# Kernel optimization log

Hardware: AMD Instinct MI355X
Metric: run time of the kernel (lower is better)

Reference implementation:

```python
import jax, jax.numpy as jnp
import numpy as np

B, N, OBJ_DIM, Q_DIM, KSIZE = 128, 36, 2048, 1024, 8
HID = Q_DIM // 2  # 512, inter_dim for obj_method='mul'
MID = Q_DIM // 4  # 256


def wn_linear(x, v, g, b):
    # weight_norm: W = g * v / ||v||_row
    w = v * (g / jnp.linalg.norm(v, axis=1))[:, None]
    return x @ w.T + b


def setup_inputs() -> dict:
    key = jax.random.key(0)
    ks = jax.random.split(key, 8)
    node_feats = jax.random.normal(ks[0], (B, N, OBJ_DIM), dtype=jnp.float32)
    q_feats = jax.random.normal(ks[1], (B, Q_DIM), dtype=jnp.float32)
    # off-diagonal (self-loops removed) flat indices into the (B*N*N,) pairwise tensor
    grid = np.arange(N * N).reshape(N, N)
    per = grid[~np.eye(N, dtype=bool)]            # (N*(N-1),)
    idx = (np.arange(B)[:, None] * (N * N) + per[None, :]).reshape(-1)
    indexes = jnp.asarray(idx, dtype=jnp.int64)
    s = 0.02
    return {
        "node_feats": node_feats,
        "q_feats": q_feats,
        "indexes": indexes,
        "v_obj": jax.random.normal(ks[2], (HID, OBJ_DIM), jnp.float32) * s,
        "g_obj": jnp.ones((HID,), jnp.float32),
        "b_obj": jnp.zeros((HID,), jnp.float32),
        "v_q": jax.random.normal(ks[3], (HID, Q_DIM), jnp.float32) * s,
        "g_q": jnp.ones((HID,), jnp.float32),
        "b_q": jnp.zeros((HID,), jnp.float32),
        "v_l1": jax.random.normal(ks[4], (MID, HID), jnp.float32) * s,
        "g_l1": jnp.ones((MID,), jnp.float32),
        "b_l1": jnp.zeros((MID,), jnp.float32),
        "v_l2": jax.random.normal(ks[5], (KSIZE, MID), jnp.float32) * s,
        "g_l2": jnp.ones((KSIZE,), jnp.float32),
        "b_l2": jnp.zeros((KSIZE,), jnp.float32),
    }


def reference(node_feats, q_feats, indexes, v_obj, g_obj, b_obj, v_q, g_q, b_q,
              v_l1, g_l1, b_l1, v_l2, g_l2, b_l2):
    b, n, _ = node_feats.shape
    nf = wn_linear(node_feats, v_obj, g_obj, b_obj)        # (b, n, HID)
    # decode flat pairwise index -> (batch, i, j); node_intersect 'mul' then gather
    bi = indexes // (n * n)
    rem = indexes % (n * n)
    i, j = rem // n, rem % n
    obj_feats = nf[bi, i] * nf[bi, j]                       # (m, HID)
    m = indexes.shape[0]
    qp = wn_linear(q_feats, v_q, g_q, b_q)                  # (b, HID)
    q_re = jnp.repeat(qp, m // b, axis=0)                   # (m, HID)
    edge_feats = obj_feats * q_re
    h = jax.nn.relu(wn_linear(edge_feats, v_l1, g_l1, b_l1))
    return wn_linear(h, v_l2, g_l2, b_l2)                   # (m, KSIZE)
```

## Files before the change

kernel.cpp:

```cpp
#include <hip/hip_runtime.h>
#include <hip/hip_fp16.h>

typedef __attribute__((ext_vector_type(8))) _Float16 half8;
typedef __attribute__((ext_vector_type(2))) __fp16 fp16x2;
typedef __attribute__((ext_vector_type(4))) float f32x4;
typedef unsigned short u16;
typedef unsigned int u32;

__device__ __forceinline__ u16 f2h(float f) {
  union { _Float16 h; u16 u; } cv; cv.h = (_Float16)f; return cv.u;
}

__device__ __forceinline__ u32 pkrtz(float a, float b) {
  union { fp16x2 h; u32 u; } cv;
  cv.h = __builtin_amdgcn_cvt_pkrtz(a, b);
  return cv.u;
}

__device__ __forceinline__ f32x4 mfma16h(half8 a, half8 b, f32x4 c) {
  return __builtin_amdgcn_mfma_f32_16x16x32_f16(a, b, c, 0, 0, 0);
}

__device__ __forceinline__ void gload_lds16(const void* g, void* l) {
  __builtin_amdgcn_global_load_lds(
      (const __attribute__((address_space(1))) void*)g,
      (__attribute__((address_space(3))) void*)l, 16, 0, 0);
}

__device__ __forceinline__ half8 ldh8(const char* p) {
  union { half8 h; int4 v; } r; r.v = *(const int4*)p; return r.h;
}

__device__ __forceinline__ uint4 pkmul4(uint4 x, uint4 y) {
  union U { uint4 v; __half2 h[4]; };
  U X, Y, E; X.v = x; Y.v = y;
  #pragma unroll
  for (int i = 0; i < 4; i++) E.h[i] = __hmul2(X.h[i], Y.h[i]);
  return E.v;
}
__device__ __forceinline__ half8 as_h8(uint4 v) {
  union { uint4 v; half8 h; } r; r.v = v; return r.h;
}

__device__ __forceinline__ void wn_row(const float* __restrict__ v,
                                       const float* __restrict__ g,
                                       int K, int Nreal, u16* __restrict__ outW,
                                       int row, int l) {
  if (row >= Nreal) {
    for (int k = l; k < K; k += 64) outW[row * K + k] = 0;
    return;
  }
  const float* vr = v + (size_t)row * K;
  float ss = 0.f;
  for (int k = l * 4; k < K; k += 256) {
    f32x4 x = *(const f32x4*)(vr + k);
    ss += x.x * x.x + x.y * x.y + x.z * x.z + x.w * x.w;
  }
  #pragma unroll
  for (int m = 32; m >= 1; m >>= 1) ss += __shfl_xor(ss, m, 64);
  const float scale = g[row] / sqrtf(ss);
  for (int k = l; k < K; k += 64) outW[row * K + k] = f2h(vr[k] * scale);
}

__global__ __launch_bounds__(256) void prep(
    const float* __restrict__ node, u16* __restrict__ node_h,
    const float* __restrict__ qf, u16* __restrict__ q_h,
    const float* __restrict__ v_obj, const float* __restrict__ g_obj,
    const float* __restrict__ v_q,   const float* __restrict__ g_q,
    const float* __restrict__ v_l1,  const float* __restrict__ g_l1,
    const float* __restrict__ v_l2,  const float* __restrict__ g_l2,
    u16* __restrict__ Wobjh, u16* __restrict__ Wqh,
    u16* __restrict__ W1f,   u16* __restrict__ W2p,
    const int* __restrict__ indexes, int* __restrict__ posPair,
    int* __restrict__ ij_tab) {
  const int b = blockIdx.x;
  if (b < 4672) {
    const int i = (b * 256 + threadIdx.x) * 8;
    const float* in; u16* out; int off;
    if (i < 9437184) { in = node; out = node_h; off = i; }
    else             { in = qf;   out = q_h;    off = i - 9437184; }
    f32x4 a = *(const f32x4*)(in + off);
    f32x4 c = *(const f32x4*)(in + off + 4);
    uint4 r;
    r.x = pkrtz(a.x, a.y); r.y = pkrtz(a.z, a.w);
    r.z = pkrtz(c.x, c.y); r.w = pkrtz(c.z, c.w);
    *(uint4*)(out + off) = r;
    return;
  }
  const int sub = threadIdx.x >> 6, l = threadIdx.x & 63;
  const int b2 = b - 4672;
  if (b2 < 128) {
    wn_row(v_obj, g_obj, 2048, 512, Wobjh, b2 * 4 + sub, l);
  } else if (b2 < 256) {
    wn_row(v_q, g_q, 1024, 512, Wqh, (b2 - 128) * 4 + sub, l);
  } else if (b2 < 320) {
    const int row = (b2 - 256) * 4 + sub;
    const float* vr = v_l1 + (size_t)row * 512;
    float ss = 0.f;
    for (int k = l * 4; k < 512; k += 256) {
      f32x4 x = *(const f32x4*)(vr + k);
      ss += x.x * x.x + x.y * x.y + x.z * x.z + x.w * x.w;
    }
    #pragma unroll
    for (int m = 32; m >= 1; m >>= 1) ss += __shfl_xor(ss, m, 64);
    const float scale = g_l1[row] / sqrtf(ss);
    const int swz = (row >> 1) & 3;
    for (int c = l; c < 512; c += 64) {
      const int kc = c >> 5, col = c & 31, q = col >> 3, e = col & 7;
      W1f[kc * 8192 + row * 32 + ((q ^ swz) << 3) + e] = f2h(vr[c] * scale);
    }
  } else if (b2 < 324) {
    wn_row(v_l2, g_l2, 256, 8, W2p, (b2 - 320) * 4 + sub, l);
  } else {
    const int m = (b2 - 324) * 256 + threadIdx.x;
    if (m < 161280) {
      const int idx = indexes[m];
      const int bi = idx / 1296;
      const int rem = idx - bi * 1296;
      const int i = rem / 36, j = rem - i * 36;
      const int i2 = (i < j) ? i : j, j2 = (i < j) ? j : i;
      const int p = i2 * (71 - i2) / 2 + (j2 - i2 - 1);
      posPair[(bi * 640 + p) * 2 + ((i < j) ? 0 : 1)] = m;
    } else {
      const int u = m - 161280;
      if (u < 1296) {
        const int i = u / 36, j = u - i * 36;
        if (i < j) ij_tab[i * (71 - i) / 2 + (j - i - 1)] = u;
      } else if (u < 1306) {
        ij_tab[630 + (u - 1296)] = 35 * 36 + 35;
      }
    }
  }
}

__global__ __launch_bounds__(256, 3) void gemm_merged(
    const u16* __restrict__ node_h, const u16* __restrict__ Wobjh,
    const float* __restrict__ b_obj, u16* __restrict__ A2h,
    const u16* __restrict__ q_h, const u16* __restrict__ Wqh,
    const float* __restrict__ b_q, u16* __restrict__ qp_h) {
  __shared__ char smem[2][24576];
  const int t = threadIdx.x, l = t & 63, w = t >> 6;
  const int lr = l & 15, lg = l >> 4;
  const int wm = w & 1, wn2 = w >> 1;

  const bool isq = (blockIdx.x == 36);
  const u16* Ab = isq ? q_h : node_h;
  const u16* Wb = isq ? Wqh : Wobjh;
  const float* bias = isq ? b_q : b_obj;
  u16* outp = isq ? qp_h : A2h;
  const int K = isq ? 1024 : 2048;
  const int nstep = isq ? 16 : 32;
  const int bm = isq ? 0 : blockIdx.x * 128;
  const int bn = blockIdx.y * 64;
  const int ldb = K * 2;

  const char* Abase = (const char*)(Ab + (size_t)bm * K);
  const char* Bbase = (const char*)(Wb + (size_t)bn * K);

  auto stage = [&](int buf, int ks) {
    const char* asrc = Abase + ks * 128;
    const char* bsrc = Bbase + ks * 128;
    #pragma unroll
    for (int it = 0; it < 4; it++) {
      const int c = it * 256 + w * 64 + l;
      const int row = c >> 3;
      const int cb = ((c & 7) * 16) ^ ((row & 7) << 4);
      gload_lds16(asrc + (size_t)row * ldb + cb, &smem[buf][(it * 256 + w * 64) * 16]);
    }
    #pragma unroll
    for (int it = 0; it < 2; it++) {
      const int c = it * 256 + w * 64 + l;
      const int row = c >> 3;
      const int cb = ((c & 7) * 16) ^ ((row & 7) << 4);
      gload_lds16(bsrc + (size_t)row * ldb + cb,
                  &smem[buf][16384 + (it * 256 + w * 64) * 16]);
    }
  };

  stage(0, 0);
  asm volatile("s_waitcnt vmcnt(0)" ::: "memory");
  __builtin_amdgcn_s_barrier();

  f32x4 acc[4][2] = {};
  for (int ks = 0; ks < nstep; ks++) {
    const int cur = ks & 1;
    if (ks + 1 < nstep) stage(cur ^ 1, ks + 1);
    const char* As = smem[cur];
    const char* Bs = smem[cur] + 16384;
    #pragma unroll
    for (int kk = 0; kk < 2; kk++) {
      half8 af[4], bf[2];
      #pragma unroll
      for (int m = 0; m < 4; m++) {
        const int r = wm * 64 + m * 16 + lr;
        af[m] = ldh8(As + r * 128 + ((kk * 64 + lg * 16) ^ ((lr & 7) << 4)));
      }
      #pragma unroll
      for (int n = 0; n < 2; n++) {
        const int r = wn2 * 32 + n * 16 + lr;
        bf[n] = ldh8(Bs + r * 128 + ((kk * 64 + lg * 16) ^ ((lr & 7) << 4)));
      }
      #pragma unroll
      for (int m = 0; m < 4; m++)
        #pragma unroll
        for (int n = 0; n < 2; n++)
          acc[m][n] = mfma16h(af[m], bf[n], acc[m][n]);
    }
    asm volatile("s_waitcnt vmcnt(0)" ::: "memory");
    __builtin_amdgcn_s_barrier();
  }

  #pragma unroll
  for (int n = 0; n < 2; n++) {
    const int c = bn + wn2 * 32 + n * 16 + lr;
    const float bv = bias[c];
    #pragma unroll
    for (int m = 0; m < 4; m++) {
      #pragma unroll
      for (int q = 0; q < 4; q++) {
        const int r = bm + wm * 64 + m * 16 + lg * 4 + q;
        outp[(size_t)r * 512 + c] = f2h(acc[m][n][q] + bv);
      }
    }
  }
}

#define OFF_QP 37440
#define OFF_W1 38464
#define EDGE_SMEM 71232

__global__ __launch_bounds__(256, 2) void edge_v11(
    const u16* __restrict__ NFg, const u16* __restrict__ QPg,
    const u16* __restrict__ W1f, const float* __restrict__ b1,
    const u16* __restrict__ W2p, const float* __restrict__ b2,
    const int* __restrict__ posPair, const int* __restrict__ ij_tab,
    float* __restrict__ out) {
  extern __shared__ char smem[];
  const int t = threadIdx.x, l = t & 63, w = t >> 6;
  const int lr = l & 15, lg = l >> 4;
  const int wm = w & 1, wn = w >> 1;
  const int bi = blockIdx.y;
  const int mb = blockIdx.x * 128;

  #pragma unroll
  for (int it = 0; it < 10; it++) {
    const int row = it * 4 + w;
    if (row < 36) {
      gload_lds16(NFg + (size_t)(bi * 36 + row) * 512 + l * 8, smem + row * 1040);
    } else if (row == 36) {
      gload_lds16(QPg + (size_t)bi * 512 + l * 8, smem + OFF_QP);
    }
  }
  #pragma unroll
  for (int it = 0; it < 4; it++) {
    gload_lds16(W1f + (size_t)(it * 256 + w * 64 + l) * 8,
                smem + OFF_W1 + (it * 256 + w * 64) * 16);
  }

  int xoff[4], yoff[4];
  #pragma unroll
  for (int m = 0; m < 4; m++) {
    const int p = mb + wm * 64 + m * 16 + lr;
    const int pij = ij_tab[p];
    const int ii = pij / 36;
    const int jj = pij - ii * 36;
    xoff[m] = ii * 1040 + lg * 16;
    yoff[m] = jj * 1040 + lg * 16;
  }
  const int qoff = OFF_QP + lg * 16;
  const int bswz = ((lr >> 1) & 3) << 4;

  asm volatile("s_waitcnt vmcnt(0)" ::: "memory");
  __builtin_amdgcn_s_barrier();

  f32x4 acc[4][8] = {};
  int cur = 0;

  for (int kc = 0; kc < 16; kc++) {
    const int nxt = cur ^ 1;
    if (kc < 15) {
      #pragma unroll
      for (int it = 0; it < 4; it++) {
        gload_lds16(W1f + (size_t)(kc + 1) * 8192 + (size_t)(it * 256 + w * 64 + l) * 8,
                    smem + OFF_W1 + nxt * 16384 + (it * 256 + w * 64) * 16);
      }
    }
    {
      const char* w1c = smem + OFF_W1 + cur * 16384;
      const int kb = kc * 64;
      const uint4 qv = *(const uint4*)(smem + qoff + kb);
      half8 bf[8];
      #pragma unroll
      for (int n = 0; n < 8; n++)
        bf[n] = ldh8(w1c + (wn * 128 + n * 16 + lr) * 64 + ((lg * 16) ^ bswz));
      #pragma unroll
      for (int m = 0; m < 4; m++) {
        uint4 x = *(const uint4*)(smem + xoff[m] + kb);
        uint4 y = *(const uint4*)(smem + yoff[m] + kb);
        half8 af = as_h8(pkmul4(pkmul4(x, y), qv));
        #pragma unroll
        for (int n = 0; n < 8; n++)
          acc[m][n] = mfma16h(af, bf[n], acc[m][n]);
      }
    }
    asm volatile("s_waitcnt vmcnt(0)" ::: "memory");
    __builtin_amdgcn_s_barrier();
    cur = nxt;
  }

  #pragma unroll
  for (int m = 0; m < 4; m++) {
    #pragma unroll
    for (int n = 0; n < 8; n++) {
      const int c = wn * 128 + n * 16 + lr;
      const float bv = b1[c];
      #pragma unroll
      for (int qq = 0; qq < 2; qq++) {
        const float v0 = fmaxf(acc[m][n][2 * qq] + bv, 0.f);
        const float v1 = fmaxf(acc[m][n][2 * qq + 1] + bv, 0.f);
        const u32 pk = pkrtz(v0, v1);
        const int r = wm * 64 + m * 16 + lg * 4 + 2 * qq;
        *(u16*)(smem + r * 528 + c * 2) = (u16)pk;
        *(u16*)(smem + (r + 1) * 528 + c * 2) = (u16)(pk >> 16);
      }
    }
  }
  __syncthreads();

  half8 w2f[8];
  #pragma unroll
  for (int kk = 0; kk < 8; kk++)
    w2f[kk] = ldh8((const char*)(W2p + lr * 256 + kk * 32 + lg * 8));

  #pragma unroll
  for (int tt = 0; tt < 2; tt++) {
    const int tile = tt * 4 + w;
    f32x4 a2c = {0.f, 0.f, 0.f, 0.f};
    #pragma unroll
    for (int kk = 0; kk < 8; kk++) {
      half8 af = ldh8(smem + (tile * 16 + lr) * 528 + kk * 64 + lg * 16);
      a2c = mfma16h(af, w2f[kk], a2c);
    }
    if (lr < 8) {
      const float b2v = b2[lr];
      #pragma unroll
      for (int q = 0; q < 4; q++) {
        const int p = mb + tile * 16 + lg * 4 + q;
        const int m0 = posPair[(bi * 640 + p) * 2];
        const int m1 = posPair[(bi * 640 + p) * 2 + 1];
        const float val = a2c[q] + b2v;
        if (m0 >= 0) out[(size_t)m0 * 8 + lr] = val;
        if (m1 >= 0) out[(size_t)m1 * 8 + lr] = val;
      }
    }
  }
}

extern "C" void kernel_launch(void* const* d_in, const int* in_sizes, int n_in,
                              void* d_out, int out_size, void* d_ws, size_t ws_size,
                              hipStream_t stream) {
  const float* node_feats = (const float*)d_in[0];
  const float* q_feats    = (const float*)d_in[1];
  const int*   indexes    = (const int*)d_in[2];
  const float* v_obj = (const float*)d_in[3];
  const float* g_obj = (const float*)d_in[4];
  const float* b_obj = (const float*)d_in[5];
  const float* v_q   = (const float*)d_in[6];
  const float* g_q   = (const float*)d_in[7];
  const float* b_q   = (const float*)d_in[8];
  const float* v_l1  = (const float*)d_in[9];
  const float* g_l1  = (const float*)d_in[10];
  const float* b_l1  = (const float*)d_in[11];
  const float* v_l2  = (const float*)d_in[12];
  const float* g_l2  = (const float*)d_in[13];
  const float* b_l2  = (const float*)d_in[14];
  float* out = (float*)d_out;

  char* ws = (char*)d_ws;
  u16*   node_h  = (u16*)(ws + 0);
  u16*   q_h     = (u16*)(ws + 18874368);
  u16*   Wobjh   = (u16*)(ws + 19136512);
  u16*   Wqh     = (u16*)(ws + 21233664);
  u16*   W1f     = (u16*)(ws + 22282240);
  u16*   W2p     = (u16*)(ws + 22544384);
  u16*   qp_h    = (u16*)(ws + 22552576);
  u16*   A2h     = (u16*)(ws + 22683648);
  int*   posPair = (int*)(ws + 27402240);
  int*   ij_tab  = (int*)(ws + 28057600);

  hipMemsetAsync(posPair, 0xFF, 655360, stream);

  prep<<<dim3(5632), dim3(256), 0, stream>>>(
      node_feats, node_h, q_feats, q_h,
      v_obj, g_obj, v_q, g_q, v_l1, g_l1, v_l2, g_l2,
      Wobjh, Wqh, W1f, W2p, indexes, posPair, ij_tab);

  gemm_merged<<<dim3(37, 8), dim3(256), 0, stream>>>(
      node_h, Wobjh, b_obj, A2h, q_h, Wqh, b_q, qp_h);

  edge_v11<<<dim3(5, 128), dim3(256), EDGE_SMEM, stream>>>(A2h, qp_h, W1f, b_l1,
                                                           W2p, b_l2, posPair, ij_tab, out);
}
```

Baseline: 94.34 us.

## Split node projection GEMM along K into two partials plus reduce kernel

The node-feature projection GEMM is split into two K halves across a third grid dimension. The doubled block count (288 to 584) is meant to fill more of the MI355X's compute units. Each half writes an fp16 partial result to a new workspace buffer, and a separate reduce kernel adds the two partials and the bias before producing A2h. The cost is an extra kernel launch, extra global memory traffic for the partials, and some precision loss from rounding each partial to fp16.

```diff
diff --git a/kernel.cpp b/kernel.cpp
--- a/kernel.cpp
+++ b/kernel.cpp
@@ -9,6 +9,10 @@
 
 __device__ __forceinline__ u16 f2h(float f) {
   union { _Float16 h; u16 u; } cv; cv.h = (_Float16)f; return cv.u;
+}
+
+__device__ __forceinline__ float h2f(u16 u) {
+  union { _Float16 h; u16 u; } cv; cv.u = u; return (float)cv.h;
 }
 
 __device__ __forceinline__ u32 pkrtz(float a, float b) {
@@ -133,29 +137,31 @@
   }
 }
 
-__global__ __launch_bounds__(256, 3) void gemm_merged(
+__global__ __launch_bounds__(256, 3) void gemm_split(
     const u16* __restrict__ node_h, const u16* __restrict__ Wobjh,
-    const float* __restrict__ b_obj, u16* __restrict__ A2h,
+    u16* __restrict__ part_h,
     const u16* __restrict__ q_h, const u16* __restrict__ Wqh,
     const float* __restrict__ b_q, u16* __restrict__ qp_h) {
+  const bool isq = (blockIdx.x == 36);
+  const int z = blockIdx.z;
+  if (isq && z == 1) return;
+
   __shared__ char smem[2][24576];
   const int t = threadIdx.x, l = t & 63, w = t >> 6;
   const int lr = l & 15, lg = l >> 4;
   const int wm = w & 1, wn2 = w >> 1;
 
-  const bool isq = (blockIdx.x == 36);
   const u16* Ab = isq ? q_h : node_h;
   const u16* Wb = isq ? Wqh : Wobjh;
-  const float* bias = isq ? b_q : b_obj;
-  u16* outp = isq ? qp_h : A2h;
   const int K = isq ? 1024 : 2048;
-  const int nstep = isq ? 16 : 32;
+  const int kbase = isq ? 0 : z * 1024;
+  const int nstep = 16;
   const int bm = isq ? 0 : blockIdx.x * 128;
   const int bn = blockIdx.y * 64;
   const int ldb = K * 2;
 
-  const char* Abase = (const char*)(Ab + (size_t)bm * K);
-  const char* Bbase = (const char*)(Wb + (size_t)bn * K);
+  const char* Abase = (const char*)(Ab + (size_t)bm * K + kbase);
+  const char* Bbase = (const char*)(Wb + (size_t)bn * K + kbase);
 
   auto stage = [&](int buf, int ks) {
     const char* asrc = Abase + ks * 128;
@@ -213,16 +219,45 @@
   #pragma unroll
   for (int n = 0; n < 2; n++) {
     const int c = bn + wn2 * 32 + n * 16 + lr;
-    const float bv = bias[c];
     #pragma unroll
     for (int m = 0; m < 4; m++) {
       #pragma unroll
       for (int q = 0; q < 4; q++) {
         const int r = bm + wm * 64 + m * 16 + lg * 4 + q;
-        outp[(size_t)r * 512 + c] = f2h(acc[m][n][q] + bv);
-      }
-    }
-  }
+        if (isq) {
+          qp_h[(size_t)r * 512 + c] = f2h(acc[m][n][q] + b_q[c]);
+        } else {
+          part_h[(size_t)z * 2359296 + (size_t)r * 512 + c] = f2h(acc[m][n][q]);
+        }
+      }
+    }
+  }
+}
+
+__global__ void nf_reduce(const u16* __restrict__ part_h,
+                          const float* __restrict__ b_obj,
+                          u16* __restrict__ A2h) {
+  const int i = (blockIdx.x * 256 + threadIdx.x) * 8;
+  union { uint4 v; __half2 h[4]; } p0, p1;
+  p0.v = *(const uint4*)(part_h + i);
+  p1.v = *(const uint4*)(part_h + 2359296 + i);
+  const int c0 = i & 511;
+  f32x4 ba = *(const f32x4*)(b_obj + c0);
+  f32x4 bb = *(const f32x4*)(b_obj + c0 + 4);
+  float s[8];
+  #pragma unroll
+  for (int k = 0; k < 4; k++) {
+    float2 a = __half22float2(p0.h[k]);
+    float2 b = __half22float2(p1.h[k]);
+    s[2 * k] = a.x + b.x;
+    s[2 * k + 1] = a.y + b.y;
+  }
+  s[0] += ba.x; s[1] += ba.y; s[2] += ba.z; s[3] += ba.w;
+  s[4] += bb.x; s[5] += bb.y; s[6] += bb.z; s[7] += bb.w;
+  uint4 r;
+  r.x = pkrtz(s[0], s[1]); r.y = pkrtz(s[2], s[3]);
+  r.z = pkrtz(s[4], s[5]); r.w = pkrtz(s[6], s[7]);
+  *(uint4*)(A2h + i) = r;
 }
 
 #define OFF_QP 37440
@@ -387,6 +422,7 @@
   u16*   A2h     = (u16*)(ws + 22683648);
   int*   posPair = (int*)(ws + 27402240);
   int*   ij_tab  = (int*)(ws + 28057600);
+  u16*   part_h  = (u16*)(ws + 28060160);
 
   hipMemsetAsync(posPair, 0xFF, 655360, stream);
 
@@ -395,8 +431,10 @@
       v_obj, g_obj, v_q, g_q, v_l1, g_l1, v_l2, g_l2,
       Wobjh, Wqh, W1f, W2p, indexes, posPair, ij_tab);
 
-  gemm_merged<<<dim3(37, 8), dim3(256), 0, stream>>>(
-      node_h, Wobjh, b_obj, A2h, q_h, Wqh, b_q, qp_h);
+  gemm_split<<<dim3(37, 8, 2), dim3(256), 0, stream>>>(
+      node_h, Wobjh, part_h, q_h, Wqh, b_q, qp_h);
+
+  nf_reduce<<<dim3(1152), dim3(256), 0, stream>>>(part_h, b_obj, A2h);
 
   edge_v11<<<dim3(5, 128), dim3(256), EDGE_SMEM, stream>>>(A2h, qp_h, W1f, b_l1,
                                                            W2p, b_l2, posPair, ij_tab, out);
```

After: 98.51 us. 1.04x slower.
